# Kernel optimization log

Measured on AMD Instinct MI355X. Metric: run time of the kernel, lower is better.

## Reference

```python
import jax, jax.numpy as jnp
import numpy as np
from functools import partial

TAU = 2.0       # membrane time constant
V_TH = 1.0      # firing threshold
SLOPE = 10.0    # surrogate sigmoid slope (matches rate_encode's 10*)
T = 10          # time_window
H = 12          # num_heads


def lif_step(v, I):
    """One LIF update: leaky integrate, surrogate spike, multiplicative reset."""
    v = v + (I - v) / TAU
    spk = jax.nn.sigmoid(SLOPE * (v - V_TH))
    v = v * (1.0 - spk)
    return spk, v


def setup_inputs() -> dict:
    key = jax.random.key(0)
    ks = jax.random.split(key, 5)
    B, S, E = 8, 1024, 768
    scale = 1.0 / np.sqrt(E)
    x = jax.random.uniform(ks[0], (B, S, E), dtype=jnp.float32)
    Wq = jax.random.normal(ks[1], (E, E), dtype=jnp.float32) * scale
    Wk = jax.random.normal(ks[2], (E, E), dtype=jnp.float32) * scale
    Wv = jax.random.normal(ks[3], (E, E), dtype=jnp.float32) * scale
    Wo = jax.random.normal(ks[4], (E, E), dtype=jnp.float32) * scale
    zb = jnp.zeros((E,), dtype=jnp.float32)
    return {"x": x, "Wq": Wq, "bq": zb, "Wk": Wk, "bk": zb,
            "Wv": Wv, "bv": zb, "Wo": Wo, "bo": zb}


def reference(x, Wq, bq, Wk, bk, Wv, bv, Wo, bo):
    B, S, E = x.shape
    D = E // H
    # rate encoding probability (x assumed in [0,1] range, clipped)
    p = jnp.clip(x, 0.0, 1.0)  # [B,S,E]

    def step(carry, t):
        vq, vk, vv, Qa, Ka, Va = carry
        inp = jax.nn.sigmoid(SLOPE * (p * T - t))  # [B,S,E] spikes at step t
        qs, vq = lif_step(vq, inp @ Wq.T + bq)
        ks, vk = lif_step(vk, inp @ Wk.T + bk)
        vs, vv = lif_step(vv, inp @ Wv.T + bv)
        return (vq, vk, vv, Qa + qs, Ka + ks, Va + vs), None

    z = jnp.zeros((B, S, E), dtype=x.dtype)
    t_idx = jnp.arange(T, dtype=x.dtype)
    (vq, vk, vv, Q, K, V), _ = jax.lax.scan(step, (z, z, z, z, z, z), t_idx)

    # split heads: [B,S,E] -> [B,H,S,D]
    Qh = Q.reshape(B, S, H, D)
    Kh = K.reshape(B, S, H, D)
    Vh = V.reshape(B, S, H, D)
    scores = jnp.einsum('bqhd,bkhd->bhqk', Qh, Kh) / np.sqrt(D)
    attn = jax.nn.softmax(scores, axis=-1)
    out_h = jnp.einsum('bhqk,bkhd->bqhd', attn, Vh)  # [B,S,H,D]
    out = out_h.reshape(B, S, E)
    # output LIF projection with fresh (zero) state
    out_spk, _ = lif_step(jnp.zeros_like(out), out @ Wo.T + bo)
    return out_spk
```

## Files before the change

kernel.cpp:

```cpp
#include <hip/hip_runtime.h>
#include <math.h>

constexpr int B_ = 8, S_ = 1024, E_ = 768, H_ = 12, D_ = 64, T_ = 10;
constexpr int N_ = B_ * S_;
constexpr int NE_ = N_ * E_;
constexpr int WE_ = E_ * E_;

typedef __attribute__((ext_vector_type(8))) short bf16x8;
typedef __attribute__((ext_vector_type(4))) float f32x4;

#define MFMA16(a,b,c) __builtin_amdgcn_mfma_f32_16x16x32_bf16(a,b,c,0,0,0)

__device__ __forceinline__ float sigm(float z){ return 1.f/(1.f+__expf(-z)); }
__device__ __forceinline__ unsigned short f2bf(float f){
    unsigned int u = __float_as_uint(f);
    u += 0x7FFFu + ((u>>16)&1u);
    return (unsigned short)(u>>16);
}
__device__ __forceinline__ float bf2f(unsigned short h){
    return __uint_as_float(((unsigned int)h)<<16);
}
__device__ __forceinline__ void gl16(const void* g, void* l){
    __builtin_amdgcn_global_load_lds((const __attribute__((address_space(1))) unsigned int*)g,
                                     (__attribute__((address_space(3))) unsigned int*)l, 16, 0, 0);
}

__global__ __launch_bounds__(256) void encode_k(const float* __restrict__ x,
                                                unsigned short* __restrict__ enc){
    const int i = blockIdx.x*256 + threadIdx.x;
    const float4 a = ((const float4*)x)[2*i];
    const float4 b = ((const float4*)x)[2*i+1];
    float p[8] = {a.x,a.y,a.z,a.w,b.x,b.y,b.z,b.w};
#pragma unroll
    for (int e=0;e<8;++e) p[e] = 100.f*fminf(fmaxf(p[e],0.f),1.f);
#pragma unroll
    for (int t=0;t<T_;++t){
        unsigned int w[4];
#pragma unroll
        for (int e=0;e<4;++e){
            unsigned short u0 = f2bf(sigm(p[2*e]   - 10.f*(float)t));
            unsigned short u1 = f2bf(sigm(p[2*e+1] - 10.f*(float)t));
            w[e] = (unsigned int)u0 | ((unsigned int)u1<<16);
        }
        ((uint4*)(enc + (long)t*NE_))[i] = make_uint4(w[0],w[1],w[2],w[3]);
    }
}

__global__ __launch_bounds__(256) void wsplit_k(const float* __restrict__ Wq, const float* __restrict__ Wk,
        const float* __restrict__ Wv, const float* __restrict__ Wo,
        unsigned short* __restrict__ whi, unsigned short* __restrict__ wlo){
    int gi = blockIdx.x*256 + threadIdx.x;
    int z = gi / (WE_/8);
    int r = gi % (WE_/8);
    const float* W = z==0?Wq : z==1?Wk : z==2?Wv : Wo;
    const float4 a = ((const float4*)W)[2*r];
    const float4 b = ((const float4*)W)[2*r+1];
    float f[8]={a.x,a.y,a.z,a.w,b.x,b.y,b.z,b.w};
    unsigned int h[4], l[4];
#pragma unroll
    for (int e=0;e<4;++e){
        unsigned short h0=f2bf(f[2*e]),   l0=f2bf(f[2*e]  -bf2f(h0));
        unsigned short h1=f2bf(f[2*e+1]), l1=f2bf(f[2*e+1]-bf2f(h1));
        h[e] = (unsigned)h0 | ((unsigned)h1<<16);
        l[e] = (unsigned)l0 | ((unsigned)l1<<16);
    }
    ((uint4*)(whi + (long)z*WE_))[r] = make_uint4(h[0],h[1],h[2],h[3]);
    ((uint4*)(wlo + (long)z*WE_))[r] = make_uint4(l[0],l[1],l[2],l[3]);
}

__global__ __launch_bounds__(256,2) void qkv_k(const unsigned short* __restrict__ enc,
        const unsigned short* __restrict__ whi,
        const float* __restrict__ bq, const float* __restrict__ bk, const float* __restrict__ bv,
        unsigned short* __restrict__ Qh_g, unsigned short* __restrict__ Ql_g,
        unsigned short* __restrict__ Kh_g, unsigned short* __restrict__ Kl_g,
        unsigned short* __restrict__ Vth_g, unsigned short* __restrict__ Vtl_g){
    const int z = blockIdx.z;
    const unsigned short* Wh = whi + (long)z*WE_;
    const float* bias = z==0?bq : z==1?bk : bv;
    const int row0 = blockIdx.x*128, col0 = blockIdx.y*64;

    __shared__ unsigned short Ab[128*64];
    __shared__ unsigned short Bh[64*64];

    const int tid = threadIdx.x, lane = tid&63, wid = tid>>6;
    const int l15 = lane&15, l4 = lane>>4, l7 = lane&7;
    const int wr = wid>>1, wc = wid&1;

    int aSrc[4], bSrc[2];
#pragma unroll
    for (int s=0;s<4;++s){
        int idx = (wid + s*4)*64 + lane;
        int row = idx>>3, ch = idx&7;
        aSrc[s] = (row0+row)*E_ + ((ch ^ (row&7))<<3);
    }
#pragma unroll
    for (int s=0;s<2;++s){
        int idx = (wid + s*4)*64 + lane;
        int row = idx>>3, ch = idx&7;
        bSrc[s] = (col0+row)*E_ + ((ch ^ (row&7))<<3);
    }

    const int aBase = (wr*64 + l15)*128;
    const int bBase = (wc*32 + l15)*128;
    const int sw[2] = { ((l4^l7)<<4), ((((4+l4))^l7)<<4) };

    f32x4 acc[4][2];
    float vm[4][2][4] = {};
    float qa[4][2][4] = {};
    float bn[2];
#pragma unroll
    for (int n=0;n<2;++n) bn[n] = bias[col0 + wc*32 + n*16 + l15];
    const f32x4 zero4 = {0.f,0.f,0.f,0.f};

    for (int t=0;t<T_;++t){
        const long tb = (long)t*NE_;
#pragma unroll
        for (int m=0;m<4;++m)
#pragma unroll
            for (int n=0;n<2;++n) acc[m][n] = zero4;
        for (int kt=0;kt<12;++kt){
            const int k0 = kt*64;
            __syncthreads();
#pragma unroll
            for (int s=0;s<4;++s)
                gl16(enc + tb + aSrc[s] + k0, &Ab[(wid+s*4)*512]);
#pragma unroll
            for (int s=0;s<2;++s)
                gl16(Wh + bSrc[s] + k0, &Bh[(wid+s*4)*512]);
            __syncthreads();
#pragma unroll
            for (int kk=0;kk<2;++kk){
                bf16x8 af[4], fbh[2];
#pragma unroll
                for (int m=0;m<4;++m)
                    af[m] = *(const bf16x8*)((const char*)Ab + aBase + m*2048 + sw[kk]);
#pragma unroll
                for (int n=0;n<2;++n)
                    fbh[n] = *(const bf16x8*)((const char*)Bh + bBase + n*2048 + sw[kk]);
#pragma unroll
                for (int m=0;m<4;++m)
#pragma unroll
                    for (int n=0;n<2;++n)
                        acc[m][n] = MFMA16(af[m], fbh[n], acc[m][n]);
            }
        }
#pragma unroll
        for (int m=0;m<4;++m)
#pragma unroll
            for (int n=0;n<2;++n)
#pragma unroll
                for (int j=0;j<4;++j){
                    float I = acc[m][n][j] + bn[n];
                    float v = (vm[m][n][j] + I)*0.5f;
                    float s = sigm(10.f*v - 10.f);
                    vm[m][n][j] = v*(1.f - s);
                    qa[m][n][j] += s;
                }
    }
    if (z == 2){
        const int b = blockIdx.x >> 3;
        const long vtb = (long)(b*12 + blockIdx.y) * 65536;
        const int keyb = (blockIdx.x & 7)*128 + wr*64 + l4*4;
#pragma unroll
        for (int m=0;m<4;++m)
#pragma unroll
            for (int n=0;n<2;++n){
                const int d = wc*32 + n*16 + l15;
                unsigned int hw[2], lw[2];
#pragma unroll
                for (int jp=0;jp<2;++jp){
                    float v0 = qa[m][n][jp*2], v1 = qa[m][n][jp*2+1];
                    unsigned short h0=f2bf(v0), h1=f2bf(v1);
                    unsigned short l0=f2bf(v0-bf2f(h0)), l1=f2bf(v1-bf2f(h1));
                    hw[jp] = (unsigned)h0 | ((unsigned)h1<<16);
                    lw[jp] = (unsigned)l0 | ((unsigned)l1<<16);
                }
                long o = vtb + (long)d*1024 + keyb + m*16;
                *(uint2*)&Vth_g[o] = make_uint2(hw[0],hw[1]);
                *(uint2*)&Vtl_g[o] = make_uint2(lw[0],lw[1]);
            }
    } else {
        unsigned short* Oh = (z==0) ? Qh_g : Kh_g;
        unsigned short* Ol = (z==0) ? Ql_g : Kl_g;
#pragma unroll
        for (int m=0;m<4;++m)
#pragma unroll
            for (int n=0;n<2;++n)
#pragma unroll
                for (int j=0;j<4;++j){
                    int row = row0 + wr*64 + m*16 + l4*4 + j;
                    int col = col0 + wc*32 + n*16 + l15;
                    float v = qa[m][n][j];
                    unsigned short hh = f2bf(v);
                    unsigned short ll = f2bf(v - bf2f(hh));
                    Oh[(long)row*E_ + col] = hh;
                    Ol[(long)row*E_ + col] = ll;
                }
    }
}

__global__ __launch_bounds__(256,2) void attn_k2(
        const unsigned short* __restrict__ Qh_g, const unsigned short* __restrict__ Ql_g,
        const unsigned short* __restrict__ Kh_g, const unsigned short* __restrict__ Kl_g,
        const unsigned short* __restrict__ Vth_g, const unsigned short* __restrict__ Vtl_g,
        unsigned short* __restrict__ atth, unsigned short* __restrict__ attl){
    const int q0 = blockIdx.x*64;
    const int h  = blockIdx.y;
    const int b  = blockIdx.z;
    const long base = ((long)b*S_)*E_ + h*64;
    const long vtb  = (long)(b*12 + h) * 65536;

    __shared__ char smem[65536];
    unsigned short* QhL = (unsigned short*)(smem);
    unsigned short* QlL = (unsigned short*)(smem + 8192);
    unsigned short* KhL = (unsigned short*)(smem + 16384);
    unsigned short* KlL = (unsigned short*)(smem + 24576);
    unsigned short* VhL = (unsigned short*)(smem + 32768);
    unsigned short* VlL = (unsigned short*)(smem + 40960);
    unsigned short* Ph = (unsigned short*)(smem + 49152);
    unsigned short* Pl = (unsigned short*)(smem + 57344);
    float* OT = (float*)(smem + 16384);

    const int tid = threadIdx.x, lane = tid&63, wid = tid>>6;
    const int l15 = lane&15, l4 = lane>>4, l7 = lane&7;
    const int qrow = wid*16 + l15;

    int sOff[2], vOff[2];
#pragma unroll
    for (int s=0;s<2;++s){
        int idx = (wid + s*4)*64 + lane;
        int r = idx>>3, c = idx&7;
        sOff[s] = r*E_ + ((c ^ (r&7))<<3);
        vOff[s] = (r<<10) + ((c ^ (r&7))<<3);
    }

#pragma unroll
    for (int s=0;s<2;++s){
        gl16(Qh_g + base + (long)q0*E_ + sOff[s], &QhL[(wid+s*4)*512]);
        gl16(Ql_g + base + (long)q0*E_ + sOff[s], &QlL[(wid+s*4)*512]);
    }
    __syncthreads();
    bf16x8 qfh[2], qfl[2];
#pragma unroll
    for (int kk=0;kk<2;++kk){
        int off = qrow*128 + ((((kk<<2)+l4) ^ l7)<<4);
        qfh[kk] = *(const bf16x8*)((const char*)QhL + off);
        qfl[kk] = *(const bf16x8*)((const char*)QlL + off);
    }

    float mrun = -1e30f, lrun = 0.f;
    f32x4 ot[4];
    const f32x4 zero4 = {0.f,0.f,0.f,0.f};
#pragma unroll
    for (int m=0;m<4;++m) ot[m] = zero4;

    for (int kt=0;kt<16;++kt){
        const int k0 = kt*64;
        __syncthreads();
#pragma unroll
        for (int s=0;s<2;++s){
            gl16(Kh_g + base + (long)k0*E_ + sOff[s], &KhL[(wid+s*4)*512]);
            gl16(Kl_g + base + (long)k0*E_ + sOff[s], &KlL[(wid+s*4)*512]);
            gl16(Vth_g + vtb + k0 + vOff[s], &VhL[(wid+s*4)*512]);
            gl16(Vtl_g + vtb + k0 + vOff[s], &VlL[(wid+s*4)*512]);
        }
        __syncthreads();
        f32x4 st[4];
#pragma unroll
        for (int m=0;m<4;++m) st[m] = zero4;
#pragma unroll
        for (int kk=0;kk<2;++kk){
            int swo = ((((kk<<2)+l4) ^ l7)<<4);
            bf16x8 kh[4], kl2[4];
#pragma unroll
            for (int m=0;m<4;++m){
                int off = (m*16+l15)*128 + swo;
                kh[m]  = *(const bf16x8*)((const char*)KhL + off);
                kl2[m] = *(const bf16x8*)((const char*)KlL + off);
            }
#pragma unroll
            for (int m=0;m<4;++m){
                st[m] = MFMA16(kh[m],  qfh[kk], st[m]);
                st[m] = MFMA16(kh[m],  qfl[kk], st[m]);
                st[m] = MFMA16(kl2[m], qfh[kk], st[m]);
            }
        }
        float pmax = -1e30f;
#pragma unroll
        for (int m=0;m<4;++m)
#pragma unroll
            for (int j=0;j<4;++j){ st[m][j] *= 0.125f; pmax = fmaxf(pmax, st[m][j]); }
        pmax = fmaxf(pmax, __shfl_xor(pmax,16));
        pmax = fmaxf(pmax, __shfl_xor(pmax,32));
        float mnew = fmaxf(mrun, pmax);
        float alpha = __expf(mrun - mnew);
        float p[16]; float psum = 0.f;
#pragma unroll
        for (int m=0;m<4;++m)
#pragma unroll
            for (int j=0;j<4;++j){ float e = __expf(st[m][j]-mnew); p[m*4+j]=e; psum+=e; }
        psum += __shfl_xor(psum,16);
        psum += __shfl_xor(psum,32);
        lrun = lrun*alpha + psum;
        mrun = mnew;
#pragma unroll
        for (int m=0;m<4;++m)
#pragma unroll
            for (int j=0;j<4;++j) ot[m][j] *= alpha;
#pragma unroll
        for (int m=0;m<4;++m)
#pragma unroll
            for (int jp=0;jp<2;++jp){
                float fx = p[m*4+jp*2], fy = p[m*4+jp*2+1];
                unsigned short hx=f2bf(fx), hy=f2bf(fy);
                unsigned short lx=f2bf(fx-bf2f(hx)), ly=f2bf(fy-bf2f(hy));
                int key = m*16 + l4*4 + jp*2;
                int byte = qrow*128 + ((key<<1) ^ (l7<<4));
                *(unsigned int*)((char*)Ph + byte) = (unsigned)hx | ((unsigned)hy<<16);
                *(unsigned int*)((char*)Pl + byte) = (unsigned)lx | ((unsigned)ly<<16);
            }
#pragma unroll
        for (int kk=0;kk<2;++kk){
            int swo = ((((kk<<2)+l4) ^ l7)<<4);
            bf16x8 pfh = *(const bf16x8*)((const char*)Ph + qrow*128 + swo);
            bf16x8 pfl = *(const bf16x8*)((const char*)Pl + qrow*128 + swo);
#pragma unroll
            for (int m=0;m<4;++m){
                int off = (m*16+l15)*128 + swo;
                bf16x8 vvh = *(const bf16x8*)((const char*)VhL + off);
                bf16x8 vvl = *(const bf16x8*)((const char*)VlL + off);
                ot[m] = MFMA16(vvh, pfh, ot[m]);
                ot[m] = MFMA16(vvh, pfl, ot[m]);
                ot[m] = MFMA16(vvl, pfh, ot[m]);
            }
        }
    }
    __syncthreads();
    float inv = 1.f/lrun;
#pragma unroll
    for (int m=0;m<4;++m)
#pragma unroll
        for (int j=0;j<4;++j){
            int d = m*16 + l4*4 + j;
            OT[qrow*68 + d] = ot[m][j]*inv;
        }
    __syncthreads();
    {
        int q = tid>>2, d0 = (tid&3)*16;
        const float* rp = OT + q*68 + d0;
        float4 f0=((const float4*)rp)[0], f1=((const float4*)rp)[1];
        float4 f2=((const float4*)rp)[2], f3=((const float4*)rp)[3];
        float f[16]={f0.x,f0.y,f0.z,f0.w,f1.x,f1.y,f1.z,f1.w,f2.x,f2.y,f2.z,f2.w,f3.x,f3.y,f3.z,f3.w};
        bf16x8 vh[2], vl[2];
#pragma unroll
        for (int g=0;g<2;++g)
#pragma unroll
            for (int e=0;e<8;++e){
                unsigned short hh = f2bf(f[g*8+e]);
                vh[g][e] = (short)hh;
                vl[g][e] = (short)f2bf(f[g*8+e]-bf2f(hh));
            }
        long o = base + (long)(q0+q)*E_ + d0;
        *(bf16x8*)(atth + o)     = vh[0];
        *(bf16x8*)(atth + o + 8) = vh[1];
        *(bf16x8*)(attl + o)     = vl[0];
        *(bf16x8*)(attl + o + 8) = vl[1];
    }
}

__global__ __launch_bounds__(256,2) void out_k(const unsigned short* __restrict__ Ah_g,
        const unsigned short* __restrict__ Al_g,
        const unsigned short* __restrict__ Wh,
        const float* __restrict__ bias, float* __restrict__ out){
    const int row0 = blockIdx.x*128, col0 = blockIdx.y*64;
    __shared__ unsigned short Ah[128*64], Al[128*64];
    __shared__ unsigned short Bh2[64*64];

    const int tid = threadIdx.x, lane = tid&63, wid = tid>>6;
    const int l15 = lane&15, l4 = lane>>4, l7 = lane&7;
    const int wr = wid>>1, wc = wid&1;

    int aSrc[4], bSrc[2];
#pragma unroll
    for (int s=0;s<4;++s){
        int idx = (wid + s*4)*64 + lane;
        int row = idx>>3, ch = idx&7;
        aSrc[s] = (row0+row)*E_ + ((ch ^ (row&7))<<3);
    }
#pragma unroll
    for (int s=0;s<2;++s){
        int idx = (wid + s*4)*64 + lane;
        int row = idx>>3, ch = idx&7;
        bSrc[s] = (col0+row)*E_ + ((ch ^ (row&7))<<3);
    }
    const int aBase = (wr*64 + l15)*128;
    const int bBase = (wc*32 + l15)*128;
    const int sw[2] = { ((l4^l7)<<4), ((((4+l4))^l7)<<4) };

    f32x4 acc[4][2];
    const f32x4 zero4 = {0.f,0.f,0.f,0.f};
#pragma unroll
    for (int m=0;m<4;++m)
#pragma unroll
        for (int n=0;n<2;++n) acc[m][n] = zero4;

    for (int kt=0;kt<12;++kt){
        const int k0 = kt*64;
        __syncthreads();
#pragma unroll
        for (int s=0;s<4;++s){
            gl16(Ah_g + aSrc[s] + k0, &Ah[(wid+s*4)*512]);
            gl16(Al_g + aSrc[s] + k0, &Al[(wid+s*4)*512]);
        }
#pragma unroll
        for (int s=0;s<2;++s)
            gl16(Wh + bSrc[s] + k0, &Bh2[(wid+s*4)*512]);
        __syncthreads();
#pragma unroll
        for (int kk=0;kk<2;++kk){
            bf16x8 ah[4], al[4], fbh[2];
#pragma unroll
            for (int m=0;m<4;++m){
                ah[m] = *(const bf16x8*)((const char*)Ah + aBase + m*2048 + sw[kk]);
                al[m] = *(const bf16x8*)((const char*)Al + aBase + m*2048 + sw[kk]);
            }
#pragma unroll
            for (int n=0;n<2;++n)
                fbh[n] = *(const bf16x8*)((const char*)Bh2 + bBase + n*2048 + sw[kk]);
#pragma unroll
            for (int m=0;m<4;++m)
#pragma unroll
                for (int n=0;n<2;++n){
                    acc[m][n] = MFMA16(ah[m], fbh[n], acc[m][n]);
                    acc[m][n] = MFMA16(al[m], fbh[n], acc[m][n]);
                }
        }
    }
#pragma unroll
    for (int m=0;m<4;++m)
#pragma unroll
        for (int n=0;n<2;++n){
            float bn = bias[col0 + wc*32 + n*16 + l15];
#pragma unroll
            for (int j=0;j<4;++j){
                int row = row0 + wr*64 + m*16 + l4*4 + j;
                int col = col0 + wc*32 + n*16 + l15;
                float I = acc[m][n][j] + bn;
                out[(long)row*E_ + col] = sigm(5.f*I - 10.f);
            }
        }
}

extern "C" void kernel_launch(void* const* d_in, const int* in_sizes, int n_in,
                              void* d_out, int out_size, void* d_ws, size_t ws_size,
                              hipStream_t stream){
    const float* x  = (const float*)d_in[0];
    const float* Wq = (const float*)d_in[1];
    const float* bq = (const float*)d_in[2];
    const float* Wk = (const float*)d_in[3];
    const float* bk = (const float*)d_in[4];
    const float* Wv = (const float*)d_in[5];
    const float* bv = (const float*)d_in[6];
    const float* Wo = (const float*)d_in[7];
    const float* bo = (const float*)d_in[8];
    float* out = (float*)d_out;

    char* ws = (char*)d_ws;
    unsigned short* enc  = (unsigned short*)ws;
    unsigned short* atth = (unsigned short*)ws;
    unsigned short* attl = (unsigned short*)(ws + (long)NE_*2);
    unsigned short* whi  = (unsigned short*)(ws + 125829120L);
    unsigned short* wlo  = whi + 4L*WE_;
    unsigned short* Qh_g  = (unsigned short*)(ws + 135266304L);
    unsigned short* Ql_g  = Qh_g + NE_;
    unsigned short* Kh_g  = Ql_g + NE_;
    unsigned short* Kl_g  = Kh_g + NE_;
    unsigned short* Vth_g = Kl_g + NE_;
    unsigned short* Vtl_g = Vth_g + NE_;

    wsplit_k<<<dim3(4*(WE_/8)/256), 256, 0, stream>>>(Wq,Wk,Wv,Wo,whi,wlo);
    encode_k<<<dim3(NE_/8/256), 256, 0, stream>>>(x,enc);
    qkv_k<<<dim3(64,12,3), 256, 0, stream>>>(enc,whi,bq,bk,bv,
                                             Qh_g,Ql_g,Kh_g,Kl_g,Vth_g,Vtl_g);
    attn_k2<<<dim3(16,12,8), 256, 0, stream>>>(Qh_g,Ql_g,Kh_g,Kl_g,Vth_g,Vtl_g,
                                               atth,attl);
    out_k<<<dim3(64,12), 256, 0, stream>>>(atth,attl,whi+3L*WE_,bo,out);
}
```

Baseline: 686.0 us.

## Move bf16 hi/lo split and V transpose out of QKV GEMM into separate kernels

```diff
diff --git a/kernel.cpp b/kernel.cpp
--- a/kernel.cpp
+++ b/kernel.cpp
@@ -71,12 +71,11 @@
 __global__ __launch_bounds__(256,2) void qkv_k(const unsigned short* __restrict__ enc,
         const unsigned short* __restrict__ whi,
         const float* __restrict__ bq, const float* __restrict__ bk, const float* __restrict__ bv,
-        unsigned short* __restrict__ Qh_g, unsigned short* __restrict__ Ql_g,
-        unsigned short* __restrict__ Kh_g, unsigned short* __restrict__ Kl_g,
-        unsigned short* __restrict__ Vth_g, unsigned short* __restrict__ Vtl_g){
+        float* __restrict__ Qf, float* __restrict__ Kf, float* __restrict__ Vf){
     const int z = blockIdx.z;
     const unsigned short* Wh = whi + (long)z*WE_;
     const float* bias = z==0?bq : z==1?bk : bv;
+    float* Out = z==0?Qf : z==1?Kf : Vf;
     const int row0 = blockIdx.x*128, col0 = blockIdx.y*64;
 
     __shared__ unsigned short Ab[128*64];
@@ -157,45 +156,78 @@
                     qa[m][n][j] += s;
                 }
     }
-    if (z == 2){
-        const int b = blockIdx.x >> 3;
-        const long vtb = (long)(b*12 + blockIdx.y) * 65536;
-        const int keyb = (blockIdx.x & 7)*128 + wr*64 + l4*4;
-#pragma unroll
-        for (int m=0;m<4;++m)
-#pragma unroll
-            for (int n=0;n<2;++n){
-                const int d = wc*32 + n*16 + l15;
-                unsigned int hw[2], lw[2];
-#pragma unroll
-                for (int jp=0;jp<2;++jp){
-                    float v0 = qa[m][n][jp*2], v1 = qa[m][n][jp*2+1];
-                    unsigned short h0=f2bf(v0), h1=f2bf(v1);
-                    unsigned short l0=f2bf(v0-bf2f(h0)), l1=f2bf(v1-bf2f(h1));
-                    hw[jp] = (unsigned)h0 | ((unsigned)h1<<16);
-                    lw[jp] = (unsigned)l0 | ((unsigned)l1<<16);
-                }
-                long o = vtb + (long)d*1024 + keyb + m*16;
-                *(uint2*)&Vth_g[o] = make_uint2(hw[0],hw[1]);
-                *(uint2*)&Vtl_g[o] = make_uint2(lw[0],lw[1]);
-            }
-    } else {
-        unsigned short* Oh = (z==0) ? Qh_g : Kh_g;
-        unsigned short* Ol = (z==0) ? Ql_g : Kl_g;
-#pragma unroll
-        for (int m=0;m<4;++m)
-#pragma unroll
-            for (int n=0;n<2;++n)
-#pragma unroll
-                for (int j=0;j<4;++j){
-                    int row = row0 + wr*64 + m*16 + l4*4 + j;
-                    int col = col0 + wc*32 + n*16 + l15;
-                    float v = qa[m][n][j];
-                    unsigned short hh = f2bf(v);
-                    unsigned short ll = f2bf(v - bf2f(hh));
-                    Oh[(long)row*E_ + col] = hh;
-                    Ol[(long)row*E_ + col] = ll;
-                }
+#pragma unroll
+    for (int m=0;m<4;++m)
+#pragma unroll
+        for (int n=0;n<2;++n)
+#pragma unroll
+            for (int j=0;j<4;++j){
+                int row = row0 + wr*64 + m*16 + l4*4 + j;
+                int col = col0 + wc*32 + n*16 + l15;
+                Out[(long)row*E_ + col] = qa[m][n][j];
+            }
+}
+
+__global__ __launch_bounds__(256) void splitqk_k(const float* __restrict__ Qf, const float* __restrict__ Kf,
+        unsigned short* __restrict__ Qh, unsigned short* __restrict__ Ql,
+        unsigned short* __restrict__ Kh, unsigned short* __restrict__ Kl){
+    const long gi = (long)blockIdx.x*256 + threadIdx.x;
+    const float* src = blockIdx.y==0 ? Qf : Kf;
+    unsigned short* oh = blockIdx.y==0 ? Qh : Kh;
+    unsigned short* ol = blockIdx.y==0 ? Ql : Kl;
+    const float4 a = ((const float4*)src)[2*gi];
+    const float4 b = ((const float4*)src)[2*gi+1];
+    float f[8]={a.x,a.y,a.z,a.w,b.x,b.y,b.z,b.w};
+    unsigned int hw[4], lw[4];
+#pragma unroll
+    for (int e=0;e<4;++e){
+        unsigned short h0=f2bf(f[2*e]),   l0=f2bf(f[2*e]  -bf2f(h0));
+        unsigned short h1=f2bf(f[2*e+1]), l1=f2bf(f[2*e+1]-bf2f(h1));
+        hw[e] = (unsigned)h0 | ((unsigned)h1<<16);
+        lw[e] = (unsigned)l0 | ((unsigned)l1<<16);
+    }
+    ((uint4*)oh)[gi] = make_uint4(hw[0],hw[1],hw[2],hw[3]);
+    ((uint4*)ol)[gi] = make_uint4(lw[0],lw[1],lw[2],lw[3]);
+}
+
+__global__ __launch_bounds__(256) void vtrans_k(const float* __restrict__ Vf,
+        unsigned short* __restrict__ Vth, unsigned short* __restrict__ Vtl){
+    __shared__ unsigned short lh[64][68], ll[64][68];
+    const int tid = threadIdx.x;
+    const long base = ((long)blockIdx.z*S_ + blockIdx.x*64)*E_ + blockIdx.y*64;
+
+    {
+        const int key = tid>>2, dq = tid&3;
+        const float* p = Vf + base + (long)key*E_ + dq*16;
+        float4 v0=((const float4*)p)[0], v1=((const float4*)p)[1];
+        float4 v2=((const float4*)p)[2], v3=((const float4*)p)[3];
+        float f[16]={v0.x,v0.y,v0.z,v0.w,v1.x,v1.y,v1.z,v1.w,
+                     v2.x,v2.y,v2.z,v2.w,v3.x,v3.y,v3.z,v3.w};
+#pragma unroll
+        for (int i=0;i<8;++i){
+            unsigned short h0=f2bf(f[2*i]),   l0=f2bf(f[2*i]  -bf2f(h0));
+            unsigned short h1=f2bf(f[2*i+1]), l1=f2bf(f[2*i+1]-bf2f(h1));
+            *(unsigned int*)&lh[key][dq*16+2*i] = (unsigned)h0 | ((unsigned)h1<<16);
+            *(unsigned int*)&ll[key][dq*16+2*i] = (unsigned)l0 | ((unsigned)l1<<16);
+        }
+    }
+    __syncthreads();
+    {
+        const int d = tid>>2, kq = tid&3;
+        unsigned int hw[8], lw[8];
+#pragma unroll
+        for (int i=0;i<8;++i){
+            unsigned short h0 = lh[kq*16+2*i][d],   h1 = lh[kq*16+2*i+1][d];
+            unsigned short l0 = ll[kq*16+2*i][d],   l1 = ll[kq*16+2*i+1][d];
+            hw[i] = (unsigned)h0 | ((unsigned)h1<<16);
+            lw[i] = (unsigned)l0 | ((unsigned)l1<<16);
+        }
+        long o = ((long)(blockIdx.z*12 + blockIdx.y))*65536 + (long)d*1024
+               + blockIdx.x*64 + kq*16;
+        ((uint4*)&Vth[o])[0] = make_uint4(hw[0],hw[1],hw[2],hw[3]);
+        ((uint4*)&Vth[o])[1] = make_uint4(hw[4],hw[5],hw[6],hw[7]);
+        ((uint4*)&Vtl[o])[0] = make_uint4(lw[0],lw[1],lw[2],lw[3]);
+        ((uint4*)&Vtl[o])[1] = make_uint4(lw[4],lw[5],lw[6],lw[7]);
     }
 }
 
@@ -469,19 +501,23 @@
     unsigned short* enc  = (unsigned short*)ws;
     unsigned short* atth = (unsigned short*)ws;
     unsigned short* attl = (unsigned short*)(ws + (long)NE_*2);
-    unsigned short* whi  = (unsigned short*)(ws + 125829120L);
-    unsigned short* wlo  = whi + 4L*WE_;
-    unsigned short* Qh_g  = (unsigned short*)(ws + 135266304L);
+    unsigned short* Qh_g  = (unsigned short*)(ws + 25165824L);
     unsigned short* Ql_g  = Qh_g + NE_;
     unsigned short* Kh_g  = Ql_g + NE_;
     unsigned short* Kl_g  = Kh_g + NE_;
     unsigned short* Vth_g = Kl_g + NE_;
     unsigned short* Vtl_g = Vth_g + NE_;
+    unsigned short* whi  = (unsigned short*)(ws + 125829120L);
+    unsigned short* wlo  = whi + 4L*WE_;
+    float* Qf = (float*)(ws + 135266304L);
+    float* Kf = Qf + NE_;
+    float* Vf = Kf + NE_;
 
     wsplit_k<<<dim3(4*(WE_/8)/256), 256, 0, stream>>>(Wq,Wk,Wv,Wo,whi,wlo);
     encode_k<<<dim3(NE_/8/256), 256, 0, stream>>>(x,enc);
-    qkv_k<<<dim3(64,12,3), 256, 0, stream>>>(enc,whi,bq,bk,bv,
-                                             Qh_g,Ql_g,Kh_g,Kl_g,Vth_g,Vtl_g);
+    qkv_k<<<dim3(64,12,3), 256, 0, stream>>>(enc,whi,bq,bk,bv,Qf,Kf,Vf);
+    splitqk_k<<<dim3(NE_/8/256, 2), 256, 0, stream>>>(Qf,Kf,Qh_g,Ql_g,Kh_g,Kl_g);
+    vtrans_k<<<dim3(16,12,8), 256, 0, stream>>>(Vf,Vth_g,Vtl_g);
     attn_k2<<<dim3(16,12,8), 256, 0, stream>>>(Qh_g,Ql_g,Kh_g,Kl_g,Vth_g,Vtl_g,
                                                atth,attl);
     out_k<<<dim3(64,12), 256, 0, stream>>>(atth,attl,whi+3L*WE_,bo,out);
```

New measurement: 585.3 us, median of 2. 14.7% less time.
